# Optimization experiments

Measured on AMD Instinct MI355X. Metric: run time of the kernel, lower is better.

Reference implementation:

```python
import jax, jax.numpy as jnp
import numpy as np

S = 5          # sample_num (fixed in source)
N = 400000     # number of splits along dim 2

def setup_inputs() -> dict:
    key = jax.random.key(0)
    k1, k2 = jax.random.split(key)
    out_matrix = jax.random.normal(k1, (S, S, N), dtype=jnp.float32)
    label_matrix = jax.random.normal(k2, (S, S, N), dtype=jnp.float32)
    return {
        "out_matrix": out_matrix,
        "label_matrix": label_matrix,
        "margin": 1,
        "sample_num": S,
    }

def reference(out_matrix, label_matrix, margin, sample_num):
    # Move split dim to front: [N, S, S]
    o = jnp.moveaxis(out_matrix, 2, 0)
    l = jnp.moveaxis(label_matrix, 2, 0)
    margin = jnp.asarray(margin, dtype=o.dtype)

    # Per split n, per row i: loss_matrix[j,k] = (o[n,i,j]-o[n,i,k]) * (l[n,i,j]-l[n,i,k])
    t1 = o[:, :, :, None] - o[:, :, None, :]   # [N, S, S, S]
    t2 = l[:, :, :, None] - l[:, :, None, :]   # [N, S, S, S]
    loss = jnp.sum(jax.nn.relu(margin - t1 * t2))

    # flat_accuracy per split: row-wise argmax agreement, summed over all splits
    pred_max = jnp.argmax(o, axis=2)    # [N, S]
    label_max = jnp.argmax(l, axis=2)   # [N, S]
    correction_num = jnp.sum(pred_max == label_max)

    return (loss, correction_num)
```

## Files before the change

### kernel.cpp

```cpp
#include <hip/hip_runtime.h>

#define SAMPLE_S 5
#define NBLOCKS  512
#define TPB      256

__device__ __forceinline__ float f4_get(const float4& v, int c) {
    switch (c) {
        case 0: return v.x;
        case 1: return v.y;
        case 2: return v.z;
        default: return v.w;
    }
}

__device__ __forceinline__ void process_row(const float ox[SAMPLE_S], const float lx[SAMPLE_S],
                                            float margin, float& loss, float& cnt) {
    int po = 0, pl = 0;
    float mo = ox[0], ml = lx[0];
#pragma unroll
    for (int j = 1; j < SAMPLE_S; ++j) {
        bool bo = ox[j] > mo;
        mo = bo ? ox[j] : mo;
        po = bo ? j : po;
        bool bl = lx[j] > ml;
        ml = bl ? lx[j] : ml;
        pl = bl ? j : pl;
    }
    if (po == pl) cnt += 1.0f;

    loss += fmaxf(margin, 0.0f) * (float)SAMPLE_S;
#pragma unroll
    for (int j = 0; j < SAMPLE_S; ++j) {
#pragma unroll
        for (int k = j + 1; k < SAMPLE_S; ++k) {
            float t = margin - (ox[j] - ox[k]) * (lx[j] - lx[k]);
            loss += 2.0f * fmaxf(t, 0.0f);
        }
    }
}

__global__ __launch_bounds__(TPB) void pml_main_kernel(
        const float* __restrict__ o, const float* __restrict__ l,
        const int* __restrict__ margin_p, float* __restrict__ ws, int N) {
    const float margin = (float)(*margin_p);
    const int b = blockIdx.x;
    const int t = threadIdx.x;

    const int C = N >> 2;
    const int q = C / NBLOCKS, r = C % NBLOCKS;
    const int cstart = b * q + (b < r ? b : r);
    const int cend   = cstart + q + (b < r ? 1 : 0);

    float loss = 0.0f, cnt = 0.0f;

    for (int c = cstart + t; c < cend; c += TPB) {
        const long long n4 = (long long)c << 2;
#pragma unroll
        for (int i = 0; i < SAMPLE_S; ++i) {
            float4 ov[SAMPLE_S], lv[SAMPLE_S];
#pragma unroll
            for (int j = 0; j < SAMPLE_S; ++j) {
                const long long base = (long long)(i * SAMPLE_S + j) * N + n4;
                ov[j] = *reinterpret_cast<const float4*>(o + base);
                lv[j] = *reinterpret_cast<const float4*>(l + base);
            }
#pragma unroll
            for (int cc = 0; cc < 4; ++cc) {
                float ox[SAMPLE_S], lx[SAMPLE_S];
#pragma unroll
                for (int j = 0; j < SAMPLE_S; ++j) {
                    ox[j] = f4_get(ov[j], cc);
                    lx[j] = f4_get(lv[j], cc);
                }
                process_row(ox, lx, margin, loss, cnt);
            }
        }
    }

    const int r4 = N & 3;
    if (b == 0 && t < r4) {
        const long long n = ((long long)C << 2) + t;
#pragma unroll
        for (int i = 0; i < SAMPLE_S; ++i) {
            float ox[SAMPLE_S], lx[SAMPLE_S];
#pragma unroll
            for (int j = 0; j < SAMPLE_S; ++j) {
                const long long idx = (long long)(i * SAMPLE_S + j) * N + n;
                ox[j] = o[idx];
                lx[j] = l[idx];
            }
            process_row(ox, lx, margin, loss, cnt);
        }
    }

#pragma unroll
    for (int off = 32; off > 0; off >>= 1) {
        loss += __shfl_down(loss, off, 64);
        cnt  += __shfl_down(cnt,  off, 64);
    }
    __shared__ float sl[TPB / 64], sc[TPB / 64];
    const int wave = t >> 6;
    const int lane = t & 63;
    if (lane == 0) { sl[wave] = loss; sc[wave] = cnt; }
    __syncthreads();
    if (t == 0) {
        float L = 0.0f, Cc = 0.0f;
#pragma unroll
        for (int w = 0; w < TPB / 64; ++w) { L += sl[w]; Cc += sc[w]; }
        ws[b]           = L;
        ws[NBLOCKS + b] = Cc;
    }
}

__global__ __launch_bounds__(NBLOCKS) void pml_reduce_kernel(
        const float* __restrict__ ws, float* __restrict__ out) {
    const int t = threadIdx.x;
    float loss = ws[t];
    float cnt  = ws[NBLOCKS + t];
#pragma unroll
    for (int off = 32; off > 0; off >>= 1) {
        loss += __shfl_down(loss, off, 64);
        cnt  += __shfl_down(cnt,  off, 64);
    }
    __shared__ float sl[NBLOCKS / 64], sc[NBLOCKS / 64];
    const int wave = t >> 6;
    const int lane = t & 63;
    if (lane == 0) { sl[wave] = loss; sc[wave] = cnt; }
    __syncthreads();
    if (t == 0) {
        float L = 0.0f, Cc = 0.0f;
#pragma unroll
        for (int w = 0; w < NBLOCKS / 64; ++w) { L += sl[w]; Cc += sc[w]; }
        out[0] = L;
        out[1] = Cc;
    }
}

extern "C" void kernel_launch(void* const* d_in, const int* in_sizes, int n_in,
                              void* d_out, int out_size, void* d_ws, size_t ws_size,
                              hipStream_t stream) {
    const float* o      = (const float*)d_in[0];
    const float* l      = (const float*)d_in[1];
    const int*   margin = (const int*)d_in[2];
    float*       out    = (float*)d_out;
    float*       ws     = (float*)d_ws;

    const int N = in_sizes[0] / (SAMPLE_S * SAMPLE_S);

    hipLaunchKernelGGL(pml_main_kernel, dim3(NBLOCKS), dim3(TPB), 0, stream,
                       o, l, margin, ws, N);
    hipLaunchKernelGGL(pml_reduce_kernel, dim3(1), dim3(NBLOCKS), 0, stream,
                       ws, out);
}
```

Baseline: 105.2 us.

## Parallelize over rows and splits with one float4 chunk per thread

Replaces the fixed 512-block grid-stride loop with a 2D grid in which each thread handles one float4 chunk of splits for a single row i (blockIdx.y). This exposes far more independent memory requests and waves to hide load latency on a bandwidth-bound kernel. Per-block partials are written as float2 and reduced by a single-block strided reduce kernel. It adds many more blocks and a longer serial tail in the reduce step.

```diff
diff --git a/kernel.cpp b/kernel.cpp
--- a/kernel.cpp
+++ b/kernel.cpp
@@ -1,8 +1,8 @@
 #include <hip/hip_runtime.h>
 
 #define SAMPLE_S 5
-#define NBLOCKS  512
 #define TPB      256
+#define RTPB     512
 
 __device__ __forceinline__ float f4_get(const float4& v, int c) {
     switch (c) {
@@ -43,45 +43,33 @@
         const float* __restrict__ o, const float* __restrict__ l,
         const int* __restrict__ margin_p, float* __restrict__ ws, int N) {
     const float margin = (float)(*margin_p);
-    const int b = blockIdx.x;
-    const int t = threadIdx.x;
-
-    const int C = N >> 2;
-    const int q = C / NBLOCKS, r = C % NBLOCKS;
-    const int cstart = b * q + (b < r ? b : r);
-    const int cend   = cstart + q + (b < r ? 1 : 0);
+    const int i = blockIdx.y;
+    const int c = blockIdx.x * TPB + threadIdx.x;
+    const long long n4 = (long long)c << 2;
+    const int bid     = blockIdx.y * gridDim.x + blockIdx.x;
 
     float loss = 0.0f, cnt = 0.0f;
 
-    for (int c = cstart + t; c < cend; c += TPB) {
-        const long long n4 = (long long)c << 2;
+    if (n4 + 3 < (long long)N) {
+        float4 ov[SAMPLE_S], lv[SAMPLE_S];
 #pragma unroll
-        for (int i = 0; i < SAMPLE_S; ++i) {
-            float4 ov[SAMPLE_S], lv[SAMPLE_S];
+        for (int j = 0; j < SAMPLE_S; ++j) {
+            const long long base = (long long)(i * SAMPLE_S + j) * N + n4;
+            ov[j] = *reinterpret_cast<const float4*>(o + base);
+            lv[j] = *reinterpret_cast<const float4*>(l + base);
+        }
+#pragma unroll
+        for (int cc = 0; cc < 4; ++cc) {
+            float ox[SAMPLE_S], lx[SAMPLE_S];
 #pragma unroll
             for (int j = 0; j < SAMPLE_S; ++j) {
-                const long long base = (long long)(i * SAMPLE_S + j) * N + n4;
-                ov[j] = *reinterpret_cast<const float4*>(o + base);
-                lv[j] = *reinterpret_cast<const float4*>(l + base);
+                ox[j] = f4_get(ov[j], cc);
+                lx[j] = f4_get(lv[j], cc);
             }
-#pragma unroll
-            for (int cc = 0; cc < 4; ++cc) {
-                float ox[SAMPLE_S], lx[SAMPLE_S];
-#pragma unroll
-                for (int j = 0; j < SAMPLE_S; ++j) {
-                    ox[j] = f4_get(ov[j], cc);
-                    lx[j] = f4_get(lv[j], cc);
-                }
-                process_row(ox, lx, margin, loss, cnt);
-            }
+            process_row(ox, lx, margin, loss, cnt);
         }
-    }
-
-    const int r4 = N & 3;
-    if (b == 0 && t < r4) {
-        const long long n = ((long long)C << 2) + t;
-#pragma unroll
-        for (int i = 0; i < SAMPLE_S; ++i) {
+    } else if (n4 < (long long)N) {
+        for (long long n = n4; n < (long long)N; ++n) {
             float ox[SAMPLE_S], lx[SAMPLE_S];
 #pragma unroll
             for (int j = 0; j < SAMPLE_S; ++j) {
@@ -99,6 +87,33 @@
         cnt  += __shfl_down(cnt,  off, 64);
     }
     __shared__ float sl[TPB / 64], sc[TPB / 64];
+    const int wave = threadIdx.x >> 6;
+    const int lane = threadIdx.x & 63;
+    if (lane == 0) { sl[wave] = loss; sc[wave] = cnt; }
+    __syncthreads();
+    if (threadIdx.x == 0) {
+        float L = 0.0f, Cc = 0.0f;
+#pragma unroll
+        for (int w = 0; w < TPB / 64; ++w) { L += sl[w]; Cc += sc[w]; }
+        reinterpret_cast<float2*>(ws)[bid] = make_float2(L, Cc);
+    }
+}
+
+__global__ __launch_bounds__(RTPB) void pml_reduce_kernel(
+        const float* __restrict__ ws, float* __restrict__ out, int nblocks) {
+    const int t = threadIdx.x;
+    float loss = 0.0f, cnt = 0.0f;
+    for (int b = t; b < nblocks; b += RTPB) {
+        float2 p = reinterpret_cast<const float2*>(ws)[b];
+        loss += p.x;
+        cnt  += p.y;
+    }
+#pragma unroll
+    for (int off = 32; off > 0; off >>= 1) {
+        loss += __shfl_down(loss, off, 64);
+        cnt  += __shfl_down(cnt,  off, 64);
+    }
+    __shared__ float sl[RTPB / 64], sc[RTPB / 64];
     const int wave = t >> 6;
     const int lane = t & 63;
     if (lane == 0) { sl[wave] = loss; sc[wave] = cnt; }
@@ -106,31 +121,7 @@
     if (t == 0) {
         float L = 0.0f, Cc = 0.0f;
 #pragma unroll
-        for (int w = 0; w < TPB / 64; ++w) { L += sl[w]; Cc += sc[w]; }
-        ws[b]           = L;
-        ws[NBLOCKS + b] = Cc;
-    }
-}
-
-__global__ __launch_bounds__(NBLOCKS) void pml_reduce_kernel(
-        const float* __restrict__ ws, float* __restrict__ out) {
-    const int t = threadIdx.x;
-    float loss = ws[t];
-    float cnt  = ws[NBLOCKS + t];
-#pragma unroll
-    for (int off = 32; off > 0; off >>= 1) {
-        loss += __shfl_down(loss, off, 64);
-        cnt  += __shfl_down(cnt,  off, 64);
-    }
-    __shared__ float sl[NBLOCKS / 64], sc[NBLOCKS / 64];
-    const int wave = t >> 6;
-    const int lane = t & 63;
-    if (lane == 0) { sl[wave] = loss; sc[wave] = cnt; }
-    __syncthreads();
-    if (t == 0) {
-        float L = 0.0f, Cc = 0.0f;
-#pragma unroll
-        for (int w = 0; w < NBLOCKS / 64; ++w) { L += sl[w]; Cc += sc[w]; }
+        for (int w = 0; w < RTPB / 64; ++w) { L += sl[w]; Cc += sc[w]; }
         out[0] = L;
         out[1] = Cc;
     }
@@ -147,8 +138,11 @@
 
     const int N = in_sizes[0] / (SAMPLE_S * SAMPLE_S);
 
-    hipLaunchKernelGGL(pml_main_kernel, dim3(NBLOCKS), dim3(TPB), 0, stream,
+    const int blocks_x = (int)(((long long)N + 4LL * TPB - 1) / (4LL * TPB));
+    const int nblocks  = blocks_x * SAMPLE_S;
+
+    hipLaunchKernelGGL(pml_main_kernel, dim3(blocks_x, SAMPLE_S), dim3(TPB), 0, stream,
                        o, l, margin, ws, N);
-    hipLaunchKernelGGL(pml_reduce_kernel, dim3(1), dim3(NBLOCKS), 0, stream,
-                       ws, out);
+    hipLaunchKernelGGL(pml_reduce_kernel, dim3(1), dim3(RTPB), 0, stream,
+                       ws, out, nblocks);
 }
```

After: 104.8 us. No clear change (-0.4%).
